# Performance work log

Hardware: AMD Instinct MI355X
Metric: run time of the kernel (lower is better)

## Reference

```python
import jax, jax.numpy as jnp
import numpy as np

L, H, V, T, E = 12, 12, 50257, 1024, 768
DH = E // H
EPS = 1e-5


def _ln(x, g, b):
    mu = jnp.mean(x, axis=-1, keepdims=True)
    var = jnp.mean(jnp.square(x - mu), axis=-1, keepdims=True)
    return g * (x - mu) * jax.lax.rsqrt(var + EPS) + b


def _gelu(x):
    # tanh-approx gelu as in the source
    return 0.5 * x * (1.0 + jnp.tanh(jnp.sqrt(2.0 / jnp.pi) * (x + 0.044715 * jnp.power(x, 3))))


def setup_inputs() -> dict:
    key = jax.random.key(0)
    ks = jax.random.split(key, 12)
    s = 0.02
    return {
        "x": jax.random.randint(ks[0], (8, T), 0, V),
        "tok_emb": jax.random.normal(ks[1], (V, E), jnp.float32) * s,
        "pos_emb": jax.random.normal(ks[2], (T, E), jnp.float32) * s,
        "ln1_g": jnp.ones((L, E), jnp.float32),
        "ln1_b": jnp.zeros((L, E), jnp.float32),
        "Wqkv": jax.random.normal(ks[3], (L, E, 3 * E), jnp.float32) * s,
        "bqkv": jnp.zeros((L, 3 * E), jnp.float32),
        "Wo": jax.random.normal(ks[4], (L, E, E), jnp.float32) * s,
        "bo": jnp.zeros((L, E), jnp.float32),
        "ln2_g": jnp.ones((L, E), jnp.float32),
        "ln2_b": jnp.zeros((L, E), jnp.float32),
        "W1": jax.random.normal(ks[5], (L, E, 4 * E), jnp.float32) * s,
        "b1": jnp.zeros((L, 4 * E), jnp.float32),
        "W2": jax.random.normal(ks[6], (L, 4 * E, E), jnp.float32) * s,
        "b2": jnp.zeros((L, E), jnp.float32),
        "lnf_g": jnp.ones((E,), jnp.float32),
        "lnf_b": jnp.zeros((E,), jnp.float32),
    }


def _gpt2(x, tok_emb, pos_emb, ln1_g, ln1_b, Wqkv, bqkv, Wo, bo,
          ln2_g, ln2_b, W1, b1, W2, b2, lnf_g, lnf_b):
    B, S = x.shape
    h = tok_emb[x] + pos_emb[:S][None, :, :]  # [B,S,E]
    mask = (jnp.arange(S)[:, None] >= jnp.arange(S)[None, :]).astype(jnp.float32)  # [S,S]
    mask = mask[None, None]  # [1,1,S,S]
    scale = jax.lax.rsqrt(jnp.float32(DH))
    for l in range(L):
        a = _ln(h, ln1_g[l], ln1_b[l])
        qkv = jnp.einsum('bse,ef->bsf', a, Wqkv[l]) + bqkv[l]
        q, k, v = jnp.split(qkv, 3, axis=-1)
        q = q.reshape(B, S, H, DH).transpose(0, 2, 1, 3)
        k = k.reshape(B, S, H, DH).transpose(0, 2, 1, 3)
        v = v.reshape(B, S, H, DH).transpose(0, 2, 1, 3)
        w = jnp.einsum('bhqd,bhkd->bhqk', q, k) * scale
        w = w * mask - 1e10 * (1.0 - mask)
        w = jax.nn.softmax(w, axis=-1)
        ctx = jnp.einsum('bhqk,bhkd->bhqd', w, v)
        ctx = ctx.transpose(0, 2, 1, 3).reshape(B, S, E)
        h = h + jnp.einsum('bse,ef->bsf', ctx, Wo[l]) + bo[l]
        a2 = _ln(h, ln2_g[l], ln2_b[l])
        ff = _gelu(jnp.einsum('bse,ef->bsf', a2, W1[l]) + b1[l])
        h = h + jnp.einsum('bsf,fe->bse', ff, W2[l]) + b2[l]
    h = _ln(h, lnf_g, lnf_b)
    last = h[:, -1, :]  # [B,E]
    return jnp.matmul(last, tok_emb.T)  # [B,V]


def reference(x, tok_emb, pos_emb, ln1_g, ln1_b, Wqkv, bqkv, Wo, bo,
              ln2_g, ln2_b, W1, b1, W2, b2, lnf_g, lnf_b):
    return _gpt2(x, tok_emb, pos_emb, ln1_g, ln1_b, Wqkv, bqkv, Wo, bo,
                 ln2_g, ln2_b, W1, b1, W2, b2, lnf_g, lnf_b)
```

## Files before the change

kernel.cpp:

```cpp
#include <hip/hip_runtime.h>
#include <math.h>

#define LNUM 12
#define HNUM 12
#define EMB 768
#define TSEQ 1024
#define BBATCH 8
#define VOCAB 50257
#define NTOK (BBATCH*TSEQ)

typedef unsigned short u16;
typedef __bf16 bf16_8 __attribute__((ext_vector_type(8)));
typedef float f32x4 __attribute__((ext_vector_type(4)));

__device__ __forceinline__ u16 f2bf(float f){
  unsigned u = __float_as_uint(f);
  u += 0x7fffu + ((u >> 16) & 1u);
  return (u16)(u >> 16);
}
__device__ __forceinline__ float wred(float v){
  #pragma unroll
  for (int m = 32; m; m >>= 1) v += __shfl_xor(v, m, 64);
  return v;
}

#define GLOAD_LDS16(g, l) \
  __builtin_amdgcn_global_load_lds((const __attribute__((address_space(1))) void*)(g), \
                                   (__attribute__((address_space(3))) void*)(l), 16, 0, 0)

template<int N> struct WCst { static constexpr int val = N; };

__global__ __launch_bounds__(256) void tcvt_kernel(const float* __restrict__ src,
                                                   u16* __restrict__ dst, int K, int N){
  __shared__ float tile[32][33];
  size_t off = (size_t)blockIdx.z * K * N;
  const float* s = src + off;
  u16* d = dst + off;
  int n0 = blockIdx.x * 32, k0 = blockIdx.y * 32;
  int tx = threadIdx.x & 31, ty = threadIdx.x >> 5;
  #pragma unroll
  for (int i = 0; i < 4; i++)
    tile[ty + i*8][tx] = s[(size_t)(k0 + ty + i*8) * N + n0 + tx];
  __syncthreads();
  #pragma unroll
  for (int i = 0; i < 4; i++){
    int n = ty + i*8;
    d[(size_t)(n0 + n) * K + k0 + tx] = f2bf(tile[tx][n]);
  }
}

__global__ __launch_bounds__(256) void embed_kernel(const int* __restrict__ x,
    const float* __restrict__ tok, const float* __restrict__ pos, float* __restrict__ h){
  int row = blockIdx.x;
  int t = row & (TSEQ - 1);
  int id = x[row];
  const float* te = tok + (size_t)id * EMB;
  const float* pe = pos + (size_t)t * EMB;
  float* hr = h + (size_t)row * EMB;
  for (int i = threadIdx.x; i < EMB; i += 256) hr[i] = te[i] + pe[i];
}

template<int OBF, int LAST>
__global__ __launch_bounds__(256) void ln_kernel(const float* __restrict__ x,
    const float* __restrict__ g, const float* __restrict__ b, void* __restrict__ out){
  int orow, row;
  if (LAST){ orow = blockIdx.x; row = blockIdx.x * TSEQ + (TSEQ - 1); }
  else     { orow = row = blockIdx.x; }
  const float* xr = x + (size_t)row * EMB;
  int tid = threadIdx.x;
  int wave = tid >> 6, lane = tid & 63;
  float v[3];
  float s = 0.f;
  #pragma unroll
  for (int i = 0; i < 3; i++){ v[i] = xr[tid + i*256]; s += v[i]; }
  __shared__ float red[4];
  s = wred(s);
  if (lane == 0) red[wave] = s;
  __syncthreads();
  float mu = (red[0] + red[1] + red[2] + red[3]) * (1.f / EMB);
  float ss = 0.f;
  #pragma unroll
  for (int i = 0; i < 3; i++){ float d = v[i] - mu; ss += d * d; }
  __syncthreads();
  ss = wred(ss);
  if (lane == 0) red[wave] = ss;
  __syncthreads();
  float var = (red[0] + red[1] + red[2] + red[3]) * (1.f / EMB);
  float rs = rsqrtf(var + 1e-5f);
  #pragma unroll
  for (int i = 0; i < 3; i++){
    int e = tid + i*256;
    float o = g[e] * (v[i] - mu) * rs + b[e];
    if (OBF) ((u16*)out)[(size_t)orow * EMB + e] = f2bf(o);
    else     ((float*)out)[(size_t)orow * EMB + e] = o;
  }
}

template<int BN, int EPI>
__global__ __launch_bounds__(512, 4) void gemm_ring(const u16* __restrict__ A,
    const u16* __restrict__ Bt, const float* __restrict__ bias,
    const float* __restrict__ resid, void* __restrict__ outp, int K, int N){
  constexpr int NB    = BN / 128;
  constexpr int LOADS = 1 + NB;
  constexpr int NWN   = BN / 64;
  constexpr int M_REP = NWN;
  constexpr int AGRP  = 8;
  constexpr int BGRP  = BN / 16;
  constexpr int SLOTE = (AGRP + BGRP) * 512;
  __shared__ __align__(16) u16 lds[3 * SLOTE];
  const int tid  = threadIdx.x;
  const int wave = tid >> 6, lane = tid & 63;
  const int q15  = lane & 15, ko = lane >> 4;
  const int wm   = wave / NWN, wn = wave % NWN;
  const int bm   = blockIdx.y, bn = blockIdx.x;
  const int NT   = K >> 5;

  const u16* gA = A  + (size_t)(bm*128 + wave*16      + q15) * K + ko * 8;
  const u16* gB = Bt + (size_t)(bn*BN  + wave*NB*16   + q15) * K + ko * 8;

#define STAGE(tt, so) do { \
    int _t = (tt); \
    GLOAD_LDS16(gA + (size_t)_t * 32, lds + (so) + wave * 512); \
    _Pragma("unroll") \
    for (int _i = 0; _i < NB; _i++) \
      GLOAD_LDS16(gB + (size_t)_i * 16 * K + (size_t)_t * 32, \
                  lds + (so) + (AGRP + wave * NB + _i) * 512); \
  } while (0)

  f32x4 acc[M_REP][4];
  #pragma unroll
  for (int i = 0; i < M_REP; i++)
    #pragma unroll
    for (int j = 0; j < 4; j++){ f32x4 z = {0.f,0.f,0.f,0.f}; acc[i][j] = z; }

  auto tile = [&](int t, int ro, int so, auto wc, bool dostage, bool dosync){
    if (dostage) STAGE(t + 2, so);
    bf16_8 af[M_REP], bfr[4];
    #pragma unroll
    for (int mi = 0; mi < M_REP; mi++)
      af[mi] = *(const bf16_8*)(lds + ro + (wm*M_REP + mi) * 512 + lane * 8);
    #pragma unroll
    for (int ni = 0; ni < 4; ni++)
      bfr[ni] = *(const bf16_8*)(lds + ro + (AGRP + wn*4 + ni) * 512 + lane * 8);
    __builtin_amdgcn_s_setprio(1);
    #pragma unroll
    for (int mi = 0; mi < M_REP; mi++)
      #pragma unroll
      for (int ni = 0; ni < 4; ni++)
        acc[mi][ni] = __builtin_amdgcn_mfma_f32_16x16x32_bf16(af[mi], bfr[ni], acc[mi][ni], 0, 0, 0);
    __builtin_amdgcn_s_setprio(0);
    if (dosync){
      asm volatile("s_waitcnt vmcnt(%0)" :: "n"(decltype(wc)::val) : "memory");
      __builtin_amdgcn_sched_barrier(0);
      __builtin_amdgcn_s_barrier();
      __builtin_amdgcn_sched_barrier(0);
    }
  };

  STAGE(0, 0);
  STAGE(1, SLOTE);
  asm volatile("s_waitcnt vmcnt(%0)" :: "n"(LOADS) : "memory");
  __builtin_amdgcn_sched_barrier(0);
  __builtin_amdgcn_s_barrier();
  __builtin_amdgcn_sched_barrier(0);

  int t = 0;
  for (; t < NT - 3; t += 3){
    tile(t,     0,         2*SLOTE, WCst<LOADS>{}, true,  true);
    tile(t + 1, SLOTE,     0,       WCst<LOADS>{}, true,  true);
    tile(t + 2, 2*SLOTE,   SLOTE,   WCst<LOADS>{}, true,  true);
  }
  tile(NT - 3, 0,       2*SLOTE, WCst<LOADS>{}, true,  true);
  tile(NT - 2, SLOTE,   0,       WCst<0>{},     false, true);
  tile(NT - 1, 2*SLOTE, 0,       WCst<0>{},     false, false);
#undef STAGE

  const int colb = bn*BN  + wn * 64;
  const int rowb = bm*128 + wm * (M_REP * 16);
  #pragma unroll
  for (int ni = 0; ni < 4; ni++){
    int col = colb + ni*16 + q15;
    float bv = bias[col];
    #pragma unroll
    for (int mi = 0; mi < M_REP; mi++){
      #pragma unroll
      for (int j = 0; j < 4; j++){
        int row = rowb + mi*16 + ko*4 + j;
        float v = acc[mi][ni][j] + bv;
        if (EPI == 1) v += resid[(size_t)row * N + col];
        if (EPI == 2){
          float y = 0.7978845608028654f * (v + 0.044715f * v * v * v);
          float e = __expf(fminf(2.f * y, 80.f));
          v = v * e / (e + 1.f);
        }
        if (EPI == 3 && col < 768) v *= 0.125f;
        if (EPI == 2 || EPI == 3) ((u16*)outp)[(size_t)row * N + col] = f2bf(v);
        else                      ((float*)outp)[(size_t)row * N + col] = v;
      }
    }
  }
}

__global__ __launch_bounds__(256) void vtrans_kernel(const u16* __restrict__ qkvb,
                                                     u16* __restrict__ vt){
  int wave = threadIdx.x >> 6, lane = threadIdx.x & 63;
  int bh = blockIdx.y, b = bh / HNUM, h = bh - b * HNUM;
  int t0 = blockIdx.x * 16 + wave * 4;
  const u16* src = qkvb + (size_t)b * TSEQ * 2304 + 1536 + h * 64 + lane;
  unsigned long long w = 0;
  #pragma unroll
  for (int i = 0; i < 4; i++)
    w |= (unsigned long long)src[(size_t)(t0 + i) * 2304] << (16 * i);
  *(unsigned long long*)(vt + ((size_t)bh * 64 + lane) * TSEQ + t0) = w;
}

__global__ __launch_bounds__(256, 2) void attn_mfma(const u16* __restrict__ qkvb,
                                                    const u16* __restrict__ vt,
                                                    u16* __restrict__ ctx){
  __shared__ u16 plds[4][64][40];
  const int wave = threadIdx.x >> 6, lane = threadIdx.x & 63;
  const int g = lane >> 4, q15 = lane & 15;
  const int bh = blockIdx.y, b = bh / HNUM, h = bh - b * HNUM;
  const int q0 = ((int)gridDim.x - 1 - (int)blockIdx.x) * 256 + wave * 64;
  const u16* qk  = qkvb + (size_t)b * TSEQ * 2304 + h * 64;
  const u16* vtb = vt + (size_t)bh * 64 * TSEQ;

#define LOADKV(kb_, kd, vd) do { \
    _Pragma("unroll") \
    for (int _kf = 0; _kf < 2; _kf++) \
      _Pragma("unroll") \
      for (int _kc = 0; _kc < 2; _kc++) \
        kd[_kf][_kc] = *(const bf16_8*)(qk + (size_t)((kb_) + _kf*16 + q15) * 2304 + 768 + _kc*32 + g*8); \
    _Pragma("unroll") \
    for (int _dc = 0; _dc < 4; _dc++) \
      vd[_dc] = *(const bf16_8*)(vtb + (size_t)(_dc*16 + q15) * TSEQ + (kb_) + g*8); \
  } while (0)

  bf16_8 qfr[4][2];
  #pragma unroll
  for (int qf = 0; qf < 4; qf++)
    #pragma unroll
    for (int kc = 0; kc < 2; kc++)
      qfr[qf][kc] = *(const bf16_8*)(qk + (size_t)(q0 + qf*16 + q15) * 2304 + kc*32 + g*8);

  f32x4 oacc[4][4];
  #pragma unroll
  for (int i = 0; i < 4; i++)
    #pragma unroll
    for (int j = 0; j < 4; j++){ f32x4 z = {0.f,0.f,0.f,0.f}; oacc[i][j] = z; }
  float mx[4] = {-1e30f,-1e30f,-1e30f,-1e30f}, lsum[4] = {0.f,0.f,0.f,0.f};

  const int kbmax = q0 + 32;
  bf16_8 kcur[2][2], vcur[4];
  LOADKV(0, kcur, vcur);

  for (int kb = 0; kb <= kbmax; kb += 32){
    bf16_8 knxt[2][2], vnxt[4];
    if (kb < kbmax) LOADKV(kb + 32, knxt, vnxt);

    f32x4 s[2][4];
    #pragma unroll
    for (int kf = 0; kf < 2; kf++)
      #pragma unroll
      for (int qf = 0; qf < 4; qf++){
        f32x4 z = {0.f,0.f,0.f,0.f};
        z = __builtin_amdgcn_mfma_f32_16x16x32_bf16(kcur[kf][0], qfr[qf][0], z, 0, 0, 0);
        z = __builtin_amdgcn_mfma_f32_16x16x32_bf16(kcur[kf][1], qfr[qf][1], z, 0, 0, 0);
        s[kf][qf] = z;
      }

    if (kb + 31 > q0){
      #pragma unroll
      for (int kf = 0; kf < 2; kf++)
        #pragma unroll
        for (int qf = 0; qf < 4; qf++)
          #pragma unroll
          for (int j = 0; j < 4; j++)
            if (kb + kf*16 + g*4 + j > q0 + qf*16 + q15) s[kf][qf][j] = -1e30f;
    }

    #pragma unroll
    for (int qf = 0; qf < 4; qf++){
      float sm = -1e30f;
      #pragma unroll
      for (int kf = 0; kf < 2; kf++)
        #pragma unroll
        for (int j = 0; j < 4; j++) sm = fmaxf(sm, s[kf][qf][j]);
      sm = fmaxf(sm, __shfl_xor(sm, 16, 64));
      sm = fmaxf(sm, __shfl_xor(sm, 32, 64));
      float mn = fmaxf(mx[qf], sm);
      float c = __expf(mx[qf] - mn);
      mx[qf] = mn;
      float ps = 0.f;
      unsigned long long pw[2];
      #pragma unroll
      for (int kf = 0; kf < 2; kf++){
        unsigned long long w = 0;
        #pragma unroll
        for (int j = 0; j < 4; j++){
          float p = __expf(s[kf][qf][j] - mn);
          ps += p;
          w |= (unsigned long long)f2bf(p) << (16 * j);
        }
        pw[kf] = w;
      }
      ps += __shfl_xor(ps, 16, 64);
      ps += __shfl_xor(ps, 32, 64);
      lsum[qf] = lsum[qf] * c + ps;
      *(unsigned long long*)&plds[wave][qf*16 + q15][g*4]      = pw[0];
      *(unsigned long long*)&plds[wave][qf*16 + q15][16 + g*4] = pw[1];
      #pragma unroll
      for (int j = 0; j < 4; j++){
        float cr = __shfl(c, g*4 + j, 64);
        #pragma unroll
        for (int dc = 0; dc < 4; dc++) oacc[qf][dc][j] *= cr;
      }
    }

    asm volatile("s_waitcnt lgkmcnt(0)" ::: "memory");
    __builtin_amdgcn_sched_barrier(0);

    bf16_8 pa[4];
    #pragma unroll
    for (int qf = 0; qf < 4; qf++)
      pa[qf] = *(const bf16_8*)&plds[wave][qf*16 + q15][g*8];
    #pragma unroll
    for (int qf = 0; qf < 4; qf++)
      #pragma unroll
      for (int dc = 0; dc < 4; dc++)
        oacc[qf][dc] = __builtin_amdgcn_mfma_f32_16x16x32_bf16(pa[qf], vcur[dc], oacc[qf][dc], 0, 0, 0);

    if (kb < kbmax){
      #pragma unroll
      for (int kf = 0; kf < 2; kf++)
        #pragma unroll
        for (int kc = 0; kc < 2; kc++) kcur[kf][kc] = knxt[kf][kc];
      #pragma unroll
      for (int dc = 0; dc < 4; dc++) vcur[dc] = vnxt[dc];
    }
  }
#undef LOADKV

  u16* cb = ctx + ((size_t)(b * TSEQ + q0)) * EMB + h * 64;
  #pragma unroll
  for (int qf = 0; qf < 4; qf++){
    float inv = 1.f / lsum[qf];
    #pragma unroll
    for (int j = 0; j < 4; j++){
      float ir = __shfl(inv, g*4 + j, 64);
      int row = qf*16 + g*4 + j;
      #pragma unroll
      for (int dc = 0; dc < 4; dc++)
        cb[(size_t)row * EMB + dc*16 + q15] = f2bf(oacc[qf][dc][j] * ir);
    }
  }
}

__global__ __launch_bounds__(256) void logits_kernel(const float* __restrict__ last,
    const float* __restrict__ tok, float* __restrict__ out){
  __shared__ float ls[BBATCH * EMB];
  for (int i = threadIdx.x; i < BBATCH * EMB; i += 256) ls[i] = last[i];
  __syncthreads();
  int wave = threadIdx.x >> 6, lane = threadIdx.x & 63;
  int v = blockIdx.x * 4 + wave;
  if (v >= VOCAB) return;
  const float* tp = tok + (size_t)v * EMB;
  float acc[BBATCH];
  #pragma unroll
  for (int b = 0; b < BBATCH; b++) acc[b] = 0.f;
  #pragma unroll
  for (int i = 0; i < EMB/64; i++){
    float tv = tp[i*64 + lane];
    #pragma unroll
    for (int b = 0; b < BBATCH; b++) acc[b] += tv * ls[b*EMB + i*64 + lane];
  }
  #pragma unroll
  for (int b = 0; b < BBATCH; b++){
    float r = wred(acc[b]);
    if (lane == 0) out[(size_t)b * VOCAB + v] = r;
  }
}

extern "C" void kernel_launch(void* const* d_in, const int* in_sizes, int n_in,
                              void* d_out, int out_size, void* d_ws, size_t ws_size,
                              hipStream_t stream){
  const int*   x    = (const int*)  d_in[0];
  const float* tok  = (const float*)d_in[1];
  const float* pos  = (const float*)d_in[2];
  const float* ln1g = (const float*)d_in[3];
  const float* ln1b = (const float*)d_in[4];
  const float* Wqkv = (const float*)d_in[5];
  const float* bqkv = (const float*)d_in[6];
  const float* Wo   = (const float*)d_in[7];
  const float* bo   = (const float*)d_in[8];
  const float* ln2g = (const float*)d_in[9];
  const float* ln2b = (const float*)d_in[10];
  const float* W1   = (const float*)d_in[11];
  const float* b1   = (const float*)d_in[12];
  const float* W2   = (const float*)d_in[13];
  const float* b2   = (const float*)d_in[14];
  const float* lnfg = (const float*)d_in[15];
  const float* lnfb = (const float*)d_in[16];

  char* p = (char*)d_ws;
  u16* wqkvT = (u16*)p;  p += (size_t)LNUM*2304*768*2;
  u16* woT   = (u16*)p;  p += (size_t)LNUM*768*768*2;
  u16* w1T   = (u16*)p;  p += (size_t)LNUM*3072*768*2;
  u16* w2T   = (u16*)p;  p += (size_t)LNUM*768*3072*2;
  float* h   = (float*)p; p += (size_t)NTOK*EMB*4;
  u16* abuf  = (u16*)p;  p += (size_t)NTOK*EMB*2;
  void* tmp  = (void*)p; p += (size_t)NTOK*2304*4;
  u16* vt    = (u16*)p;  p += (size_t)BBATCH*HNUM*64*TSEQ*2;
  float* lastb = (float*)p; p += (size_t)BBATCH*EMB*4;
  if (ws_size < (size_t)(p - (char*)d_ws)) return;

  tcvt_kernel<<<dim3(2304/32, 768/32, LNUM), 256, 0, stream>>>(Wqkv, wqkvT, 768, 2304);
  tcvt_kernel<<<dim3(768/32,  768/32, LNUM), 256, 0, stream>>>(Wo,   woT,   768, 768);
  tcvt_kernel<<<dim3(3072/32, 768/32, LNUM), 256, 0, stream>>>(W1,   w1T,   768, 3072);
  tcvt_kernel<<<dim3(768/32, 3072/32, LNUM), 256, 0, stream>>>(W2,   w2T,   3072, 768);
  embed_kernel<<<NTOK, 256, 0, stream>>>(x, tok, pos, h);

  u16* qkvb = (u16*)tmp;
  u16* ff   = (u16*)tmp;
  for (int l = 0; l < LNUM; l++){
    ln_kernel<1,0><<<NTOK, 256, 0, stream>>>(h, ln1g + l*EMB, ln1b + l*EMB, abuf);
    gemm_ring<256,3><<<dim3(2304/256, NTOK/128), 512, 0, stream>>>(
        abuf, wqkvT + (size_t)l*2304*768, bqkv + (size_t)l*2304, nullptr, qkvb, 768, 2304);
    vtrans_kernel<<<dim3(TSEQ/16, BBATCH*HNUM), 256, 0, stream>>>(qkvb, vt);
    attn_mfma<<<dim3(TSEQ/256, BBATCH*HNUM), 256, 0, stream>>>(qkvb, vt, abuf);
    gemm_ring<128,1><<<dim3(768/128, NTOK/128), 512, 0, stream>>>(
        abuf, woT + (size_t)l*768*768, bo + (size_t)l*768, h, h, 768, 768);
    ln_kernel<1,0><<<NTOK, 256, 0, stream>>>(h, ln2g + l*EMB, ln2b + l*EMB, abuf);
    gemm_ring<256,2><<<dim3(3072/256, NTOK/128), 512, 0, stream>>>(
        abuf, w1T + (size_t)l*3072*768, b1 + (size_t)l*3072, nullptr, ff, 768, 3072);
    gemm_ring<128,1><<<dim3(768/128, NTOK/128), 512, 0, stream>>>(
        ff, w2T + (size_t)l*768*3072, b2 + (size_t)l*768, h, h, 3072, 768);
  }
  ln_kernel<0,1><<<BBATCH, 256, 0, stream>>>(h, lnfg, lnfb, lastb);
  logits_kernel<<<(VOCAB + 3)/4, 256, 0, stream>>>(lastb, tok, (float*)d_out);
}
```

Baseline: 4.555 ms.

## Use uniform 128x128 GEMM tiles with 4 waves and XCD-aware block remapping

Replaces the templated BN GEMM (512 threads, 128xBN tiles) with a single 128x128 tile kernel of 256 threads, where each wave computes a 64x64 subtile with 4x4 MFMA accumulators. It also switches to a 1D grid whose block index is remapped so consecutive tiles land on the same XCD, aiming at better L2 reuse of A/B panels. The larger per-wave tile raises register use and changes the occupancy target (launch bounds 256,3). The remap assumes the grid size is divisible by 8.

```diff
diff --git a/kernel.cpp b/kernel.cpp
--- a/kernel.cpp
+++ b/kernel.cpp
@@ -96,55 +96,52 @@
   }
 }
 
-template<int BN, int EPI>
-__global__ __launch_bounds__(512, 4) void gemm_ring(const u16* __restrict__ A,
+template<int EPI>
+__global__ __launch_bounds__(256, 3) void gemm_ring(const u16* __restrict__ A,
     const u16* __restrict__ Bt, const float* __restrict__ bias,
     const float* __restrict__ resid, void* __restrict__ outp, int K, int N){
-  constexpr int NB    = BN / 128;
-  constexpr int LOADS = 1 + NB;
-  constexpr int NWN   = BN / 64;
-  constexpr int M_REP = NWN;
-  constexpr int AGRP  = 8;
-  constexpr int BGRP  = BN / 16;
-  constexpr int SLOTE = (AGRP + BGRP) * 512;
+  constexpr int SLOTE = 16 * 512;
+  constexpr int LOADS = 4;
   __shared__ __align__(16) u16 lds[3 * SLOTE];
   const int tid  = threadIdx.x;
   const int wave = tid >> 6, lane = tid & 63;
   const int q15  = lane & 15, ko = lane >> 4;
-  const int wm   = wave / NWN, wn = wave % NWN;
-  const int bm   = blockIdx.y, bn = blockIdx.x;
-  const int NT   = K >> 5;
-
-  const u16* gA = A  + (size_t)(bm*128 + wave*16      + q15) * K + ko * 8;
-  const u16* gB = Bt + (size_t)(bn*BN  + wave*NB*16   + q15) * K + ko * 8;
+  const int wm   = wave >> 1, wn = wave & 1;
+  const int nwg = (int)gridDim.x, cpx = nwg >> 3, d = (int)blockIdx.x;
+  const int orig = (d & 7) * cpx + (d >> 3);
+  const int NBN = N >> 7;
+  const int bn = orig % NBN, bm = orig / NBN;
+  const int NT = K >> 5;
+
+  const u16* gA = A  + (size_t)(bm*128 + wave*16 + q15) * K + ko * 8;
+  const u16* gB = Bt + (size_t)(bn*128 + wave*16 + q15) * K + ko * 8;
 
 #define STAGE(tt, so) do { \
     int _t = (tt); \
-    GLOAD_LDS16(gA + (size_t)_t * 32, lds + (so) + wave * 512); \
-    _Pragma("unroll") \
-    for (int _i = 0; _i < NB; _i++) \
-      GLOAD_LDS16(gB + (size_t)_i * 16 * K + (size_t)_t * 32, \
-                  lds + (so) + (AGRP + wave * NB + _i) * 512); \
+    GLOAD_LDS16(gA + (size_t)_t*32,                 lds + (so) + wave*512); \
+    GLOAD_LDS16(gA + (size_t)_t*32 + (size_t)64*K,  lds + (so) + (wave+4)*512); \
+    GLOAD_LDS16(gB + (size_t)_t*32,                 lds + (so) + (8+wave)*512); \
+    GLOAD_LDS16(gB + (size_t)_t*32 + (size_t)64*K,  lds + (so) + (12+wave)*512); \
   } while (0)
 
-  f32x4 acc[M_REP][4];
-  #pragma unroll
-  for (int i = 0; i < M_REP; i++)
+  f32x4 acc[4][4];
+  #pragma unroll
+  for (int i = 0; i < 4; i++)
     #pragma unroll
     for (int j = 0; j < 4; j++){ f32x4 z = {0.f,0.f,0.f,0.f}; acc[i][j] = z; }
 
   auto tile = [&](int t, int ro, int so, auto wc, bool dostage, bool dosync){
     if (dostage) STAGE(t + 2, so);
-    bf16_8 af[M_REP], bfr[4];
-    #pragma unroll
-    for (int mi = 0; mi < M_REP; mi++)
-      af[mi] = *(const bf16_8*)(lds + ro + (wm*M_REP + mi) * 512 + lane * 8);
+    bf16_8 af[4], bfr[4];
+    #pragma unroll
+    for (int mi = 0; mi < 4; mi++)
+      af[mi] = *(const bf16_8*)(lds + ro + (wm*4 + mi) * 512 + lane * 8);
     #pragma unroll
     for (int ni = 0; ni < 4; ni++)
-      bfr[ni] = *(const bf16_8*)(lds + ro + (AGRP + wn*4 + ni) * 512 + lane * 8);
+      bfr[ni] = *(const bf16_8*)(lds + ro + (8 + wn*4 + ni) * 512 + lane * 8);
     __builtin_amdgcn_s_setprio(1);
     #pragma unroll
-    for (int mi = 0; mi < M_REP; mi++)
+    for (int mi = 0; mi < 4; mi++)
       #pragma unroll
       for (int ni = 0; ni < 4; ni++)
         acc[mi][ni] = __builtin_amdgcn_mfma_f32_16x16x32_bf16(af[mi], bfr[ni], acc[mi][ni], 0, 0, 0);
@@ -164,25 +161,24 @@
   __builtin_amdgcn_s_barrier();
   __builtin_amdgcn_sched_barrier(0);
 
-  int t = 0;
-  for (; t < NT - 3; t += 3){
-    tile(t,     0,         2*SLOTE, WCst<LOADS>{}, true,  true);
-    tile(t + 1, SLOTE,     0,       WCst<LOADS>{}, true,  true);
-    tile(t + 2, 2*SLOTE,   SLOTE,   WCst<LOADS>{}, true,  true);
+  for (int t = 0; t < NT - 3; t += 3){
+    tile(t,     0,       2*SLOTE, WCst<LOADS>{}, true,  true);
+    tile(t + 1, SLOTE,   0,       WCst<LOADS>{}, true,  true);
+    tile(t + 2, 2*SLOTE, SLOTE,   WCst<LOADS>{}, true,  true);
   }
   tile(NT - 3, 0,       2*SLOTE, WCst<LOADS>{}, true,  true);
   tile(NT - 2, SLOTE,   0,       WCst<0>{},     false, true);
   tile(NT - 1, 2*SLOTE, 0,       WCst<0>{},     false, false);
 #undef STAGE
 
-  const int colb = bn*BN  + wn * 64;
-  const int rowb = bm*128 + wm * (M_REP * 16);
+  const int colb = bn*128 + wn*64;
+  const int rowb = bm*128 + wm*64;
   #pragma unroll
   for (int ni = 0; ni < 4; ni++){
     int col = colb + ni*16 + q15;
     float bv = bias[col];
     #pragma unroll
-    for (int mi = 0; mi < M_REP; mi++){
+    for (int mi = 0; mi < 4; mi++){
       #pragma unroll
       for (int j = 0; j < 4; j++){
         int row = rowb + mi*16 + ko*4 + j;
@@ -424,16 +420,16 @@
   u16* ff   = (u16*)tmp;
   for (int l = 0; l < LNUM; l++){
     ln_kernel<1,0><<<NTOK, 256, 0, stream>>>(h, ln1g + l*EMB, ln1b + l*EMB, abuf);
-    gemm_ring<256,3><<<dim3(2304/256, NTOK/128), 512, 0, stream>>>(
+    gemm_ring<3><<<(2304/128)*(NTOK/128), 256, 0, stream>>>(
         abuf, wqkvT + (size_t)l*2304*768, bqkv + (size_t)l*2304, nullptr, qkvb, 768, 2304);
     vtrans_kernel<<<dim3(TSEQ/16, BBATCH*HNUM), 256, 0, stream>>>(qkvb, vt);
     attn_mfma<<<dim3(TSEQ/256, BBATCH*HNUM), 256, 0, stream>>>(qkvb, vt, abuf);
-    gemm_ring<128,1><<<dim3(768/128, NTOK/128), 512, 0, stream>>>(
+    gemm_ring<1><<<(768/128)*(NTOK/128), 256, 0, stream>>>(
         abuf, woT + (size_t)l*768*768, bo + (size_t)l*768, h, h, 768, 768);
     ln_kernel<1,0><<<NTOK, 256, 0, stream>>>(h, ln2g + l*EMB, ln2b + l*EMB, abuf);
-    gemm_ring<256,2><<<dim3(3072/256, NTOK/128), 512, 0, stream>>>(
+    gemm_ring<2><<<(3072/128)*(NTOK/128), 256, 0, stream>>>(
         abuf, w1T + (size_t)l*3072*768, b1 + (size_t)l*3072, nullptr, ff, 768, 3072);
-    gemm_ring<128,1><<<dim3(768/128, NTOK/128), 512, 0, stream>>>(
+    gemm_ring<1><<<(768/128)*(NTOK/128), 256, 0, stream>>>(
         ff, w2T + (size_t)l*768*3072, b2 + (size_t)l*768, h, h, 3072, 768);
   }
   ln_kernel<0,1><<<BBATCH, 256, 0, stream>>>(h, lnfg, lnfb, lastb);
```

New measurement: 4.570 ms. About the same (+0.3%).
